# Optimization experiments

Measured on AMD Instinct MI355X. Metric: run time of the kernel, lower is better.

The kernel has to match this reference:

```python
import jax, jax.numpy as jnp
import numpy as np

N_NODES = 100000
N_EDGES = 1600000
IN_F, HID, N_COLORS = 128, 128, 10


def setup_inputs() -> dict:
    key = jax.random.key(0)
    k1, k2, k3, k4 = jax.random.split(key, 4)
    x = jax.random.normal(k1, (N_NODES, IN_F), dtype=jnp.float32)
    edge_index = jax.random.randint(k2, (2, N_EDGES), 0, N_NODES, dtype=jnp.int64)
    # Glorot-ish init for weights
    W1 = jax.random.normal(k3, (IN_F, HID), dtype=jnp.float32) / np.sqrt(IN_F)
    b1 = jnp.zeros((HID,), dtype=jnp.float32)
    W2 = jax.random.normal(k4, (HID, N_COLORS), dtype=jnp.float32) / np.sqrt(HID)
    b2 = jnp.zeros((N_COLORS,), dtype=jnp.float32)
    return {"x": x, "edge_index": edge_index, "W1": W1, "b1": b1, "W2": W2, "b2": b2}


def _gcn_norm(edge_index, num_nodes):
    # Add self-loops, compute symmetric normalization D^-1/2 (A+I) D^-1/2
    loops = jnp.arange(num_nodes, dtype=edge_index.dtype)
    src = jnp.concatenate([edge_index[0], loops])
    dst = jnp.concatenate([edge_index[1], loops])
    deg = jax.ops.segment_sum(jnp.ones_like(dst, dtype=jnp.float32), dst,
                              num_segments=num_nodes)
    deg_isqrt = jax.lax.rsqrt(deg)  # deg >= 1 due to self-loops
    norm = deg_isqrt[src] * deg_isqrt[dst]  # [E + N]
    return src, dst, norm


def _gcn_conv(h, src, dst, norm, num_nodes, W, b):
    # Linear transform first (PyG GCNConv), then gather-scale-scatter aggregate
    h = h @ W                                   # [N, out]
    msg = h[src] * norm[:, None]                # [E + N, out] gather
    out = jax.ops.segment_sum(msg, dst, num_segments=num_nodes)  # scatter-add
    return out + b


def reference(x, edge_index, W1, b1, W2, b2):
    n = x.shape[0]
    src, dst, norm = _gcn_norm(edge_index, n)
    h = _gcn_conv(x, src, dst, norm, n, W1, b1)
    h = jax.nn.relu(h)
    # dropout is identity in eval mode
    h = _gcn_conv(h, src, dst, norm, n, W2, b2)
    return jax.nn.softmax(h, axis=1)
```

## Files before the change

### kernel.cpp

```cpp
#include <hip/hip_runtime.h>
#include <hip/hip_fp16.h>

#define IN_F 128
#define HID  128
#define NC   10
#define H2P  16
#define NPB  128
#define NBMAX 784
#define BCAP 2560
#define CAPP 2944
#define EPB  4096
#define LDW  136

typedef _Float16 f16x8 __attribute__((ext_vector_type(8)));
typedef float f32x4 __attribute__((ext_vector_type(4)));
typedef int int4a __attribute__((ext_vector_type(4), aligned(4)));

__device__ inline __half2 shfl_xor_h2(__half2 v, int mask) {
    int i = __shfl_xor(*reinterpret_cast<int*>(&v), mask, 64);
    return *reinterpret_cast<__half2*>(&i);
}

__global__ __launch_bounds__(1024) void k_bin(const int* __restrict__ src,
                                              const int* __restrict__ dst,
                                              int* __restrict__ bcnt,
                                              unsigned int* __restrict__ binned,
                                              const float* __restrict__ W1,
                                              __half* __restrict__ WT,
                                              const float* __restrict__ W2,
                                              float* __restrict__ W2T,
                                              int E, int nbin) {
    __shared__ int hist[NBMAX];
    __shared__ int base[NBMAX];
    __shared__ int lofs[NBMAX];
    __shared__ int lcur[NBMAX];
    __shared__ int scan[1024];
    __shared__ unsigned int stage[EPB];
    __shared__ unsigned short sbin[EPB];
    const int tid = threadIdx.x;

    if (blockIdx.x == 0) {
        for (int i = tid; i < IN_F * HID; i += 1024) {
            int k = i >> 7, n = i & 127;
            WT[n * IN_F + k] = __float2half(W1[k * HID + n]);
        }
        for (int i = tid; i < NC * IN_F; i += 1024)
            W2T[i] = W2[(i & 127) * NC + (i >> 7)];
    }

    for (int b = tid; b < nbin; b += 1024) { hist[b] = 0; lcur[b] = 0; }
    __syncthreads();

    const int e0 = blockIdx.x * EPB + tid;
    int d[4], s[4];
    #pragma unroll
    for (int u = 0; u < 4; u++) {
        int e = e0 + u * 1024;
        d[u] = (e < E) ? dst[e] : -1;
        s[u] = (e < E) ? src[e] : 0;
        if (d[u] >= 0) atomicAdd(&hist[d[u] >> 7], 1);
    }
    __syncthreads();
    for (int b = tid; b < nbin; b += 1024) {
        int h = hist[b];
        base[b] = h ? atomicAdd(&bcnt[b], h) : 0;
    }
    scan[tid] = (tid < nbin) ? hist[tid] : 0;
    __syncthreads();
    for (int off = 1; off < 1024; off <<= 1) {
        int t = (tid >= off) ? scan[tid - off] : 0;
        __syncthreads();
        scan[tid] += t;
        __syncthreads();
    }
    if (tid < nbin) lofs[tid] = scan[tid] - hist[tid];
    __syncthreads();
    #pragma unroll
    for (int u = 0; u < 4; u++) {
        if (d[u] >= 0) {
            int b = d[u] >> 7;
            int slot = lofs[b] + atomicAdd(&lcur[b], 1);
            stage[slot] = ((unsigned)(d[u] & 127) << 17) | (unsigned)s[u];
            sbin[slot] = (unsigned short)b;
        }
    }
    __syncthreads();
    const int total = scan[1023];
    for (int i = tid; i < total; i += 1024) {
        int b = sbin[i];
        int o = base[b] + (i - lofs[b]);
        if (o < BCAP) binned[(size_t)b * BCAP + o] = stage[i];
    }
}

__global__ __launch_bounds__(512) void k_pg(const int* __restrict__ bcnt,
                                            const unsigned int* __restrict__ binned,
                                            int2* __restrict__ rowinfo,
                                            float* __restrict__ dis,
                                            int* __restrict__ csr,
                                            const float* __restrict__ X,
                                            const __half* __restrict__ WT,
                                            __half* __restrict__ hsh,
                                            __half* __restrict__ h2h,
                                            int N) {
    __shared__ int h[NPB];
    __shared__ int lb[NPB];
    __shared__ int cur[NPB];
    __shared__ float sdis[NPB];
    __shared__ int wtot[2];
    __shared__ _Float16 sX[2][32 * LDW];
    __shared__ _Float16 sW[128 * LDW];
    const int b = blockIdx.x;
    const int tid = threadIdx.x;

    if (tid < NPB) h[tid] = 0;
    __syncthreads();

    const int m = min(bcnt[b], BCAP);
    const unsigned int* p = binned + (size_t)b * BCAP;
    for (int i = tid; i < m; i += 512) atomicAdd(&h[p[i] >> 17], 1);
    __syncthreads();

    int myh = 0, cnt4 = 0;
    if (tid < NPB) { myh = h[tid]; cnt4 = (myh + 3) & ~3; }
    int inc = cnt4;
    if (tid < NPB) {
        #pragma unroll
        for (int off = 1; off < 64; off <<= 1) {
            int t = __shfl_up(inc, off, 64);
            if ((tid & 63) >= off) inc += t;
        }
        if ((tid & 63) == 63) wtot[tid >> 6] = inc;
    }
    __syncthreads();
    int ex = 0;
    if (tid < NPB) {
        ex = inc - cnt4 + ((tid >= 64) ? wtot[0] : 0);
        int node = b * NPB + tid;
        if (node < N) {
            rowinfo[node] = make_int2(b * CAPP + ex, cnt4);
            float dd = rsqrtf(1.0f + (float)myh);
            dis[node] = dd;
            sdis[tid] = dd;
        }
        lb[tid] = ex;
        cur[tid] = 0;
    }
    __syncthreads();
    for (int i = tid; i < m; i += 512) {
        unsigned v = p[i];
        int dl = v >> 17;
        int r = atomicAdd(&cur[dl], 1);
        csr[b * CAPP + lb[dl] + r] = (int)(v & 0x1FFFF);
    }
    if (tid < NPB) {
        for (int k = myh; k < cnt4; k++) csr[b * CAPP + ex + k] = N;
    }
    if (b == 0) {
        f16x8 z = {0, 0, 0, 0, 0, 0, 0, 0};
        if (tid < 16) *(f16x8*)(hsh + (size_t)N * HID + tid * 8) = z;
        if (tid < 2)  *(f16x8*)(h2h + (size_t)N * H2P + tid * 8) = z;
    }

    {
        int n = tid >> 2, part = tid & 3;
        const f16x8* srcp = (const f16x8*)(WT + n * IN_F);
        f16x8* dstp = (f16x8*)(sW + n * LDW);
        #pragma unroll
        for (int c = 0; c < 4; c++) dstp[part * 4 + c] = srcp[part * 4 + c];
    }

    const int wave = tid >> 6;
    const int grp  = wave >> 2;
    const int nbase = (wave & 3) * 32;
    const int lane = tid & 63;
    const int quad = lane >> 4;
    const int l16 = lane & 15;
    const int sub256 = tid >> 8;
    const int t256 = tid & 255;

    for (int t = 0; t < 2; t++) {
        __syncthreads();
        {
            int tdx = 2 * t + sub256;
            int r = t256 >> 3;
            int k0 = (t256 & 7) * 16;
            int row = b * NPB + tdx * 32 + r;
            if (row >= N) row = N - 1;
            const float* sp = X + (size_t)row * IN_F + k0;
            float4 f0 = *(const float4*)(sp);
            float4 f1 = *(const float4*)(sp + 4);
            float4 f2 = *(const float4*)(sp + 8);
            float4 f3 = *(const float4*)(sp + 12);
            f16x8 h0, h1;
            h0[0] = (_Float16)f0.x; h0[1] = (_Float16)f0.y;
            h0[2] = (_Float16)f0.z; h0[3] = (_Float16)f0.w;
            h0[4] = (_Float16)f1.x; h0[5] = (_Float16)f1.y;
            h0[6] = (_Float16)f1.z; h0[7] = (_Float16)f1.w;
            h1[0] = (_Float16)f2.x; h1[1] = (_Float16)f2.y;
            h1[2] = (_Float16)f2.z; h1[3] = (_Float16)f2.w;
            h1[4] = (_Float16)f3.x; h1[5] = (_Float16)f3.y;
            h1[6] = (_Float16)f3.z; h1[7] = (_Float16)f3.w;
            *(f16x8*)(sX[sub256] + r * LDW + k0) = h0;
            *(f16x8*)(sX[sub256] + r * LDW + k0 + 8) = h1;
        }
        __syncthreads();

        const int tdx = 2 * t + grp;
        f32x4 acc00 = {0,0,0,0}, acc01 = {0,0,0,0}, acc10 = {0,0,0,0}, acc11 = {0,0,0,0};
        #pragma unroll
        for (int kc = 0; kc < 4; kc++) {
            const int koff = kc * 32 + quad * 8;
            f16x8 a0 = *(const f16x8*)(sX[grp] + l16 * LDW + koff);
            f16x8 a1 = *(const f16x8*)(sX[grp] + (16 + l16) * LDW + koff);
            f16x8 b0 = *(const f16x8*)(sW + (nbase + l16) * LDW + koff);
            f16x8 b1 = *(const f16x8*)(sW + (nbase + 16 + l16) * LDW + koff);
            acc00 = __builtin_amdgcn_mfma_f32_16x16x32_f16(a0, b0, acc00, 0, 0, 0);
            acc01 = __builtin_amdgcn_mfma_f32_16x16x32_f16(a0, b1, acc01, 0, 0, 0);
            acc10 = __builtin_amdgcn_mfma_f32_16x16x32_f16(a1, b0, acc10, 0, 0, 0);
            acc11 = __builtin_amdgcn_mfma_f32_16x16x32_f16(a1, b1, acc11, 0, 0, 0);
        }
        #pragma unroll
        for (int r = 0; r < 4; r++) {
            {
                int lr = tdx * 32 + quad * 4 + r;
                int row = b * NPB + lr;
                if (row < N) {
                    float d = sdis[lr];
                    __half* o = hsh + (size_t)row * HID + nbase + l16;
                    o[0]  = __float2half(acc00[r] * d);
                    o[16] = __float2half(acc01[r] * d);
                }
            }
            {
                int lr = tdx * 32 + 16 + quad * 4 + r;
                int row = b * NPB + lr;
                if (row < N) {
                    float d = sdis[lr];
                    __half* o = hsh + (size_t)row * HID + nbase + l16;
                    o[0]  = __float2half(acc10[r] * d);
                    o[16] = __float2half(acc11[r] * d);
                }
            }
        }
    }
}

__global__ __launch_bounds__(256) void k_agg1(const __half* __restrict__ hsh,
                                              const int2* __restrict__ rowinfo,
                                              const int* __restrict__ csr,
                                              const float* __restrict__ dis,
                                              const float* __restrict__ b1,
                                              const float* __restrict__ W2T,
                                              __half* __restrict__ h2h,
                                              int N) {
    const int node = blockIdx.x * 4 + (threadIdx.x >> 6);
    if (node >= N) return;
    const int lane = threadIdx.x & 63;
    const int g   = lane >> 4;
    const int l16 = lane & 15;
    const int f0  = l16 * 8;
    const __half2 hz = __half2half2(__float2half(0.0f));

    const int2 ri = rowinfo[node];
    const int beg = ri.x, end = ri.x + ri.y;
    const float d = dis[node];

    __half2 acc2[4] = {hz, hz, hz, hz};
    if (g == 0) {
        float4 r = *(const float4*)(hsh + (size_t)node * HID + f0);
        const __half2* hh = (const __half2*)&r;
        acc2[0] = hh[0]; acc2[1] = hh[1]; acc2[2] = hh[2]; acc2[3] = hh[3];
    }

    int j0 = beg + 4 * g;
    if (j0 < end) {
        int4a cv0 = *(const int4a*)(csr + j0);
        int  j1 = j0 + 16;
        bool m1 = j1 < end;
        int4a cv1 = m1 ? *(const int4a*)(csr + j1) : cv0;
        float4 r0 = *(const float4*)(hsh + (size_t)cv0[0] * HID + f0);
        float4 r1 = *(const float4*)(hsh + (size_t)cv0[1] * HID + f0);
        float4 r2 = *(const float4*)(hsh + (size_t)cv0[2] * HID + f0);
        float4 r3 = *(const float4*)(hsh + (size_t)cv0[3] * HID + f0);
        while (true) {
            const int  j2 = j1 + 16;
            const bool m2 = m1 && (j2 < end);
            int4a cv2 = m2 ? *(const int4a*)(csr + j2) : cv1;
            float4 n0, n1, n2, n3;
            if (m1) {
                n0 = *(const float4*)(hsh + (size_t)cv1[0] * HID + f0);
                n1 = *(const float4*)(hsh + (size_t)cv1[1] * HID + f0);
                n2 = *(const float4*)(hsh + (size_t)cv1[2] * HID + f0);
                n3 = *(const float4*)(hsh + (size_t)cv1[3] * HID + f0);
            }
            const __half2* h0 = (const __half2*)&r0;
            const __half2* h1 = (const __half2*)&r1;
            const __half2* h2 = (const __half2*)&r2;
            const __half2* h3 = (const __half2*)&r3;
            #pragma unroll
            for (int i = 0; i < 4; i++) {
                acc2[i] = __hadd2(acc2[i], h0[i]);
                acc2[i] = __hadd2(acc2[i], h1[i]);
                acc2[i] = __hadd2(acc2[i], h2[i]);
                acc2[i] = __hadd2(acc2[i], h3[i]);
            }
            if (!m1) break;
            r0 = n0; r1 = n1; r2 = n2; r3 = n3;
            cv1 = cv2; m1 = m2; j1 = j2;
        }
    }

    #pragma unroll
    for (int i = 0; i < 4; i++) {
        acc2[i] = __hadd2(acc2[i], shfl_xor_h2(acc2[i], 16));
        acc2[i] = __hadd2(acc2[i], shfl_xor_h2(acc2[i], 32));
    }
    float acc[8];
    #pragma unroll
    for (int i = 0; i < 4; i++) {
        float2 t = __half22float2(acc2[i]);
        acc[2 * i] = t.x; acc[2 * i + 1] = t.y;
    }

    float4 ba = *(const float4*)(b1 + f0);
    float4 bb = *(const float4*)(b1 + f0 + 4);
    float h[8];
    h[0] = fmaxf(fmaf(d, acc[0], ba.x), 0.0f);
    h[1] = fmaxf(fmaf(d, acc[1], ba.y), 0.0f);
    h[2] = fmaxf(fmaf(d, acc[2], ba.z), 0.0f);
    h[3] = fmaxf(fmaf(d, acc[3], ba.w), 0.0f);
    h[4] = fmaxf(fmaf(d, acc[4], bb.x), 0.0f);
    h[5] = fmaxf(fmaf(d, acc[5], bb.y), 0.0f);
    h[6] = fmaxf(fmaf(d, acc[6], bb.z), 0.0f);
    h[7] = fmaxf(fmaf(d, acc[7], bb.w), 0.0f);

    const int cb = (g == 0) ? 0 : (g == 1) ? 3 : (g == 2) ? 6 : 8;
    const int nc = (g < 2) ? 3 : 2;
    float p[3];
    #pragma unroll
    for (int ci = 0; ci < 3; ci++) {
        if (ci < nc) {
            int c = cb + ci;
            float4 wa = *(const float4*)(W2T + c * IN_F + f0);
            float4 wb = *(const float4*)(W2T + c * IN_F + f0 + 4);
            float t = fmaf(h[0], wa.x, fmaf(h[1], wa.y, fmaf(h[2], wa.z, h[3] * wa.w)));
            t = fmaf(h[4], wb.x, fmaf(h[5], wb.y, fmaf(h[6], wb.z, fmaf(h[7], wb.w, t))));
            #pragma unroll
            for (int off = 1; off < 16; off <<= 1) t += __shfl_xor(t, off, 64);
            p[ci] = t;
        }
    }
    if (l16 == 0) {
        __half* o = h2h + (size_t)node * H2P + cb;
        for (int ci = 0; ci < nc; ci++) o[ci] = __float2half(d * p[ci]);
    }
}

__global__ __launch_bounds__(256) void k_agg2(const __half* __restrict__ h2h,
                                              const int2* __restrict__ rowinfo,
                                              const int* __restrict__ csr,
                                              const float* __restrict__ dis,
                                              const float* __restrict__ b2,
                                              float* __restrict__ out,
                                              int N) {
    int t = blockIdx.x * 256 + threadIdx.x;
    int node = t >> 3;
    if (node >= N) return;
    int o = t & 7;
    int q = o & 1;
    int eg = o >> 1;
    const int base = q * 8;
    const __half2 hz = __half2half2(__float2half(0.0f));

    __half2 a2[4] = {hz, hz, hz, hz};
    if (eg == 0) {
        float4 r = *(const float4*)(h2h + (size_t)node * H2P + base);
        const __half2* hh = (const __half2*)&r;
        a2[0] = hh[0]; a2[1] = hh[1]; a2[2] = hh[2]; a2[3] = hh[3];
    }
    const int2 ri = rowinfo[node];
    const int end = ri.x + ri.y;

    int j0 = ri.x + 4 * eg;
    if (j0 < end) {
        int4a cv0 = *(const int4a*)(csr + j0);
        int  j1 = j0 + 16;
        bool m1 = j1 < end;
        int4a cv1 = m1 ? *(const int4a*)(csr + j1) : cv0;
        float4 r0 = *(const float4*)(h2h + (size_t)cv0[0] * H2P + base);
        float4 r1 = *(const float4*)(h2h + (size_t)cv0[1] * H2P + base);
        float4 r2 = *(const float4*)(h2h + (size_t)cv0[2] * H2P + base);
        float4 r3 = *(const float4*)(h2h + (size_t)cv0[3] * H2P + base);
        while (true) {
            const int  j2 = j1 + 16;
            const bool m2 = m1 && (j2 < end);
            int4a cv2 = m2 ? *(const int4a*)(csr + j2) : cv1;
            float4 n0, n1, n2, n3;
            if (m1) {
                n0 = *(const float4*)(h2h + (size_t)cv1[0] * H2P + base);
                n1 = *(const float4*)(h2h + (size_t)cv1[1] * H2P + base);
                n2 = *(const float4*)(h2h + (size_t)cv1[2] * H2P + base);
                n3 = *(const float4*)(h2h + (size_t)cv1[3] * H2P + base);
            }
            const __half2* h0 = (const __half2*)&r0;
            const __half2* h1 = (const __half2*)&r1;
            const __half2* h2 = (const __half2*)&r2;
            const __half2* h3 = (const __half2*)&r3;
            #pragma unroll
            for (int i = 0; i < 4; i++) {
                a2[i] = __hadd2(a2[i], h0[i]);
                a2[i] = __hadd2(a2[i], h1[i]);
                a2[i] = __hadd2(a2[i], h2[i]);
                a2[i] = __hadd2(a2[i], h3[i]);
            }
            if (!m1) break;
            r0 = n0; r1 = n1; r2 = n2; r3 = n3;
            cv1 = cv2; m1 = m2; j1 = j2;
        }
    }

    #pragma unroll
    for (int i = 0; i < 4; i++) {
        a2[i] = __hadd2(a2[i], shfl_xor_h2(a2[i], 2));
        a2[i] = __hadd2(a2[i], shfl_xor_h2(a2[i], 4));
    }

    float a[8];
    #pragma unroll
    for (int i = 0; i < 4; i++) {
        float2 tt = __half22float2(a2[i]);
        a[2 * i] = tt.x; a[2 * i + 1] = tt.y;
    }

    const float d = dis[node];
    float vv[8];
    #pragma unroll
    for (int i = 0; i < 8; i++) {
        int f = base + i;
        vv[i] = (f < NC) ? fmaf(d, a[i], b2[f]) : -1e30f;
    }
    float m = vv[0];
    #pragma unroll
    for (int i = 1; i < 8; i++) m = fmaxf(m, vv[i]);
    m = fmaxf(m, __shfl_xor(m, 1, 64));
    float e[8];
    float s = 0.0f;
    #pragma unroll
    for (int i = 0; i < 8; i++) { e[i] = (base + i < NC) ? expf(vv[i] - m) : 0.0f; s += e[i]; }
    s += __shfl_xor(s, 1, 64);
    float inv = 1.0f / s;

    float* op = out + (size_t)node * NC;
    if (o == 0) {
        *(float2*)(op + 0) = make_float2(e[0] * inv, e[1] * inv);
        *(float2*)(op + 2) = make_float2(e[2] * inv, e[3] * inv);
        *(float2*)(op + 4) = make_float2(e[4] * inv, e[5] * inv);
        *(float2*)(op + 6) = make_float2(e[6] * inv, e[7] * inv);
    } else if (o == 1) {
        *(float2*)(op + 8) = make_float2(e[0] * inv, e[1] * inv);
    }
}

extern "C" void kernel_launch(void* const* d_in, const int* in_sizes, int n_in,
                              void* d_out, int out_size, void* d_ws, size_t ws_size,
                              hipStream_t stream) {
    const float* x  = (const float*)d_in[0];
    const int*   ei = (const int*)d_in[1];
    const float* W1 = (const float*)d_in[2];
    const float* b1 = (const float*)d_in[3];
    const float* W2 = (const float*)d_in[4];
    const float* b2 = (const float*)d_in[5];
    float* out = (float*)d_out;

    const int N = in_sizes[0] / IN_F;
    const int E = in_sizes[1] / 2;
    const int* esrc = ei;
    const int* edst = ei + E;
    const int nbin = (N + NPB - 1) / NPB;

    char* ws = (char*)d_ws;
    int2*   rowinfo = (int2*)(ws);
    float*  dis     = (float*)(ws + 0x100000);
    int*    bcnt    = (int*)(ws + 0x180000);
    __half* WT      = (__half*)(ws + 0x190000);
    float*  W2T     = (float*)(ws + 0x1A0000);
    unsigned int* binned = (unsigned int*)(ws + 0x200000);
    int*    csr     = (int*)(ws + 0xA00000);
    __half* hsh     = (__half*)(ws + 0x1400000);
    __half* h2h     = (__half*)(ws + 0x2D00000);

    hipMemsetAsync(bcnt, 0, (size_t)nbin * sizeof(int), stream);

    k_bin <<<(E + EPB - 1) / EPB, 1024, 0, stream>>>(esrc, edst, bcnt, binned, W1, WT, W2, W2T, E, nbin);
    k_pg  <<<nbin, 512, 0, stream>>>(bcnt, binned, rowinfo, dis, csr, x, WT, hsh, h2h, N);
    k_agg1<<<(N + 3) / 4, 256, 0, stream>>>(hsh, rowinfo, csr, dis, b1, W2T, h2h, N);
    k_agg2<<<(int)(((size_t)N * 8 + 255) / 256), 256, 0, stream>>>(h2h, rowinfo, csr, dis, b2, out, N);
}
```

Before: 224.5 us.

## Use wave-shuffle scan in binning and widen projection kernel to 1024 threads

In the binning kernel, the 1024-entry shared-memory Hillis-Steele scan with many barriers is replaced by a two-level wavefront shuffle scan. Edge indices are now loaded as int4 vectors with contiguous per-thread edges. The gather/projection kernel moves to 1024 threads per block, so all four 32-row X tiles are staged at once and the two-iteration loop with its barriers is removed. The binned entries are also kept in registers between the histogram and CSR-fill passes instead of being reloaded. The cost is a larger block, which raises per-block LDS and register use, lowers occupancy, and assumes at most 3072 entries per bin.

```diff
diff --git a/kernel.cpp b/kernel.cpp
--- a/kernel.cpp
+++ b/kernel.cpp
@@ -34,7 +34,7 @@
     __shared__ int base[NBMAX];
     __shared__ int lofs[NBMAX];
     __shared__ int lcur[NBMAX];
-    __shared__ int scan[1024];
+    __shared__ int wsum[16];
     __shared__ unsigned int stage[EPB];
     __shared__ unsigned short sbin[EPB];
     const int tid = threadIdx.x;
@@ -51,30 +51,52 @@
     for (int b = tid; b < nbin; b += 1024) { hist[b] = 0; lcur[b] = 0; }
     __syncthreads();
 
-    const int e0 = blockIdx.x * EPB + tid;
+    const int e0 = blockIdx.x * EPB + tid * 4;
     int d[4], s[4];
-    #pragma unroll
-    for (int u = 0; u < 4; u++) {
-        int e = e0 + u * 1024;
-        d[u] = (e < E) ? dst[e] : -1;
-        s[u] = (e < E) ? src[e] : 0;
+    if (e0 + 3 < E) {
+        int4a dv = *(const int4a*)(dst + e0);
+        int4a sv = *(const int4a*)(src + e0);
+        d[0] = dv[0]; d[1] = dv[1]; d[2] = dv[2]; d[3] = dv[3];
+        s[0] = sv[0]; s[1] = sv[1]; s[2] = sv[2]; s[3] = sv[3];
+    } else {
+        #pragma unroll
+        for (int u = 0; u < 4; u++) {
+            d[u] = (e0 + u < E) ? dst[e0 + u] : -1;
+            s[u] = (e0 + u < E) ? src[e0 + u] : 0;
+        }
+    }
+    #pragma unroll
+    for (int u = 0; u < 4; u++)
         if (d[u] >= 0) atomicAdd(&hist[d[u] >> 7], 1);
-    }
-    __syncthreads();
+    __syncthreads();
+
     for (int b = tid; b < nbin; b += 1024) {
         int h = hist[b];
         base[b] = h ? atomicAdd(&bcnt[b], h) : 0;
     }
-    scan[tid] = (tid < nbin) ? hist[tid] : 0;
-    __syncthreads();
-    for (int off = 1; off < 1024; off <<= 1) {
-        int t = (tid >= off) ? scan[tid - off] : 0;
-        __syncthreads();
-        scan[tid] += t;
-        __syncthreads();
-    }
-    if (tid < nbin) lofs[tid] = scan[tid] - hist[tid];
-    __syncthreads();
+    int v = (tid < nbin) ? hist[tid] : 0;
+    int inc = v;
+    #pragma unroll
+    for (int off = 1; off < 64; off <<= 1) {
+        int t = __shfl_up(inc, off, 64);
+        if ((tid & 63) >= off) inc += t;
+    }
+    if ((tid & 63) == 63) wsum[tid >> 6] = inc;
+    __syncthreads();
+    if (tid < 64) {
+        int wv = (tid < 16) ? wsum[tid] : 0;
+        int winc = wv;
+        #pragma unroll
+        for (int off = 1; off < 16; off <<= 1) {
+            int t = __shfl_up(winc, off, 64);
+            if (tid >= off) winc += t;
+        }
+        if (tid < 16) wsum[tid] = winc - wv;
+    }
+    __syncthreads();
+    if (tid < nbin) lofs[tid] = inc - v + wsum[tid >> 6];
+    __syncthreads();
+
     #pragma unroll
     for (int u = 0; u < 4; u++) {
         if (d[u] >= 0) {
@@ -85,7 +107,7 @@
         }
     }
     __syncthreads();
-    const int total = scan[1023];
+    const int total = lofs[nbin - 1] + hist[nbin - 1];
     for (int i = tid; i < total; i += 1024) {
         int b = sbin[i];
         int o = base[b] + (i - lofs[b]);
@@ -93,22 +115,22 @@
     }
 }
 
-__global__ __launch_bounds__(512) void k_pg(const int* __restrict__ bcnt,
-                                            const unsigned int* __restrict__ binned,
-                                            int2* __restrict__ rowinfo,
-                                            float* __restrict__ dis,
-                                            int* __restrict__ csr,
-                                            const float* __restrict__ X,
-                                            const __half* __restrict__ WT,
-                                            __half* __restrict__ hsh,
-                                            __half* __restrict__ h2h,
-                                            int N) {
+__global__ __launch_bounds__(1024) void k_pg(const int* __restrict__ bcnt,
+                                             const unsigned int* __restrict__ binned,
+                                             int2* __restrict__ rowinfo,
+                                             float* __restrict__ dis,
+                                             int* __restrict__ csr,
+                                             const float* __restrict__ X,
+                                             const __half* __restrict__ WT,
+                                             __half* __restrict__ hsh,
+                                             __half* __restrict__ h2h,
+                                             int N) {
     __shared__ int h[NPB];
     __shared__ int lb[NPB];
     __shared__ int cur[NPB];
     __shared__ float sdis[NPB];
     __shared__ int wtot[2];
-    __shared__ _Float16 sX[2][32 * LDW];
+    __shared__ _Float16 sX[4][32 * LDW];
     __shared__ _Float16 sW[128 * LDW];
     const int b = blockIdx.x;
     const int tid = threadIdx.x;
@@ -118,7 +140,11 @@
 
     const int m = min(bcnt[b], BCAP);
     const unsigned int* p = binned + (size_t)b * BCAP;
-    for (int i = tid; i < m; i += 512) atomicAdd(&h[p[i] >> 17], 1);
+    const int i0 = tid, i1 = tid + 1024, i2 = tid + 2048;
+    unsigned pv0 = 0, pv1 = 0, pv2 = 0;
+    if (i0 < m) { pv0 = p[i0]; atomicAdd(&h[pv0 >> 17], 1); }
+    if (i1 < m) { pv1 = p[i1]; atomicAdd(&h[pv1 >> 17], 1); }
+    if (i2 < m) { pv2 = p[i2]; atomicAdd(&h[pv2 >> 17], 1); }
     __syncthreads();
 
     int myh = 0, cnt4 = 0;
@@ -147,12 +173,9 @@
         cur[tid] = 0;
     }
     __syncthreads();
-    for (int i = tid; i < m; i += 512) {
-        unsigned v = p[i];
-        int dl = v >> 17;
-        int r = atomicAdd(&cur[dl], 1);
-        csr[b * CAPP + lb[dl] + r] = (int)(v & 0x1FFFF);
-    }
+    if (i0 < m) { int dl = pv0 >> 17; int r = atomicAdd(&cur[dl], 1); csr[b * CAPP + lb[dl] + r] = (int)(pv0 & 0x1FFFF); }
+    if (i1 < m) { int dl = pv1 >> 17; int r = atomicAdd(&cur[dl], 1); csr[b * CAPP + lb[dl] + r] = (int)(pv1 & 0x1FFFF); }
+    if (i2 < m) { int dl = pv2 >> 17; int r = atomicAdd(&cur[dl], 1); csr[b * CAPP + lb[dl] + r] = (int)(pv2 & 0x1FFFF); }
     if (tid < NPB) {
         for (int k = myh; k < cnt4; k++) csr[b * CAPP + ex + k] = N;
     }
@@ -163,12 +186,37 @@
     }
 
     {
-        int n = tid >> 2, part = tid & 3;
+        int n = tid >> 3, c = tid & 7;
         const f16x8* srcp = (const f16x8*)(WT + n * IN_F);
         f16x8* dstp = (f16x8*)(sW + n * LDW);
-        #pragma unroll
-        for (int c = 0; c < 4; c++) dstp[part * 4 + c] = srcp[part * 4 + c];
-    }
+        dstp[c]     = srcp[c];
+        dstp[c + 8] = srcp[c + 8];
+    }
+    {
+        const int sub = tid >> 8;
+        const int t256 = tid & 255;
+        const int r = t256 >> 3;
+        const int k0 = (t256 & 7) * 16;
+        int row = b * NPB + sub * 32 + r;
+        if (row >= N) row = N - 1;
+        const float* sp = X + (size_t)row * IN_F + k0;
+        float4 f0 = *(const float4*)(sp);
+        float4 f1 = *(const float4*)(sp + 4);
+        float4 f2 = *(const float4*)(sp + 8);
+        float4 f3 = *(const float4*)(sp + 12);
+        f16x8 h0, h1;
+        h0[0] = (_Float16)f0.x; h0[1] = (_Float16)f0.y;
+        h0[2] = (_Float16)f0.z; h0[3] = (_Float16)f0.w;
+        h0[4] = (_Float16)f1.x; h0[5] = (_Float16)f1.y;
+        h0[6] = (_Float16)f1.z; h0[7] = (_Float16)f1.w;
+        h1[0] = (_Float16)f2.x; h1[1] = (_Float16)f2.y;
+        h1[2] = (_Float16)f2.z; h1[3] = (_Float16)f2.w;
+        h1[4] = (_Float16)f3.x; h1[5] = (_Float16)f3.y;
+        h1[6] = (_Float16)f3.z; h1[7] = (_Float16)f3.w;
+        *(f16x8*)(sX[sub] + r * LDW + k0) = h0;
+        *(f16x8*)(sX[sub] + r * LDW + k0 + 8) = h1;
+    }
+    __syncthreads();
 
     const int wave = tid >> 6;
     const int grp  = wave >> 2;
@@ -176,71 +224,40 @@
     const int lane = tid & 63;
     const int quad = lane >> 4;
     const int l16 = lane & 15;
-    const int sub256 = tid >> 8;
-    const int t256 = tid & 255;
-
-    for (int t = 0; t < 2; t++) {
-        __syncthreads();
+
+    f32x4 acc00 = {0,0,0,0}, acc01 = {0,0,0,0}, acc10 = {0,0,0,0}, acc11 = {0,0,0,0};
+    #pragma unroll
+    for (int kc = 0; kc < 4; kc++) {
+        const int koff = kc * 32 + quad * 8;
+        f16x8 a0 = *(const f16x8*)(sX[grp] + l16 * LDW + koff);
+        f16x8 a1 = *(const f16x8*)(sX[grp] + (16 + l16) * LDW + koff);
+        f16x8 b0 = *(const f16x8*)(sW + (nbase + l16) * LDW + koff);
+        f16x8 b1 = *(const f16x8*)(sW + (nbase + 16 + l16) * LDW + koff);
+        acc00 = __builtin_amdgcn_mfma_f32_16x16x32_f16(a0, b0, acc00, 0, 0, 0);
+        acc01 = __builtin_amdgcn_mfma_f32_16x16x32_f16(a0, b1, acc01, 0, 0, 0);
+        acc10 = __builtin_amdgcn_mfma_f32_16x16x32_f16(a1, b0, acc10, 0, 0, 0);
+        acc11 = __builtin_amdgcn_mfma_f32_16x16x32_f16(a1, b1, acc11, 0, 0, 0);
+    }
+    #pragma unroll
+    for (int r = 0; r < 4; r++) {
         {
-            int tdx = 2 * t + sub256;
-            int r = t256 >> 3;
-            int k0 = (t256 & 7) * 16;
-            int row = b * NPB + tdx * 32 + r;
-            if (row >= N) row = N - 1;
-            const float* sp = X + (size_t)row * IN_F + k0;
-            float4 f0 = *(const float4*)(sp);
-            float4 f1 = *(const float4*)(sp + 4);
-            float4 f2 = *(const float4*)(sp + 8);
-            float4 f3 = *(const float4*)(sp + 12);
-            f16x8 h0, h1;
-            h0[0] = (_Float16)f0.x; h0[1] = (_Float16)f0.y;
-            h0[2] = (_Float16)f0.z; h0[3] = (_Float16)f0.w;
-            h0[4] = (_Float16)f1.x; h0[5] = (_Float16)f1.y;
-            h0[6] = (_Float16)f1.z; h0[7] = (_Float16)f1.w;
-            h1[0] = (_Float16)f2.x; h1[1] = (_Float16)f2.y;
-            h1[2] = (_Float16)f2.z; h1[3] = (_Float16)f2.w;
-            h1[4] = (_Float16)f3.x; h1[5] = (_Float16)f3.y;
-            h1[6] = (_Float16)f3.z; h1[7] = (_Float16)f3.w;
-            *(f16x8*)(sX[sub256] + r * LDW + k0) = h0;
-            *(f16x8*)(sX[sub256] + r * LDW + k0 + 8) = h1;
-        }
-        __syncthreads();
-
-        const int tdx = 2 * t + grp;
-        f32x4 acc00 = {0,0,0,0}, acc01 = {0,0,0,0}, acc10 = {0,0,0,0}, acc11 = {0,0,0,0};
-        #pragma unroll
-        for (int kc = 0; kc < 4; kc++) {
-            const int koff = kc * 32 + quad * 8;
-            f16x8 a0 = *(const f16x8*)(sX[grp] + l16 * LDW + koff);
-            f16x8 a1 = *(const f16x8*)(sX[grp] + (16 + l16) * LDW + koff);
-            f16x8 b0 = *(const f16x8*)(sW + (nbase + l16) * LDW + koff);
-            f16x8 b1 = *(const f16x8*)(sW + (nbase + 16 + l16) * LDW + koff);
-            acc00 = __builtin_amdgcn_mfma_f32_16x16x32_f16(a0, b0, acc00, 0, 0, 0);
-            acc01 = __builtin_amdgcn_mfma_f32_16x16x32_f16(a0, b1, acc01, 0, 0, 0);
-            acc10 = __builtin_amdgcn_mfma_f32_16x16x32_f16(a1, b0, acc10, 0, 0, 0);
-            acc11 = __builtin_amdgcn_mfma_f32_16x16x32_f16(a1, b1, acc11, 0, 0, 0);
-        }
-        #pragma unroll
-        for (int r = 0; r < 4; r++) {
-            {
-                int lr = tdx * 32 + quad * 4 + r;
-                int row = b * NPB + lr;
-                if (row < N) {
-                    float d = sdis[lr];
-                    __half* o = hsh + (size_t)row * HID + nbase + l16;
-                    o[0]  = __float2half(acc00[r] * d);
-                    o[16] = __float2half(acc01[r] * d);
-                }
+            int lr = grp * 32 + quad * 4 + r;
+            int row = b * NPB + lr;
+            if (row < N) {
+                float d = sdis[lr];
+                __half* o = hsh + (size_t)row * HID + nbase + l16;
+                o[0]  = __float2half(acc00[r] * d);
+                o[16] = __float2half(acc01[r] * d);
             }
-            {
-                int lr = tdx * 32 + 16 + quad * 4 + r;
-                int row = b * NPB + lr;
-                if (row < N) {
-                    float d = sdis[lr];
-                    __half* o = hsh + (size_t)row * HID + nbase + l16;
-                    o[0]  = __float2half(acc10[r] * d);
-                    o[16] = __float2half(acc11[r] * d);
-                }
+        }
+        {
+            int lr = grp * 32 + 16 + quad * 4 + r;
+            int row = b * NPB + lr;
+            if (row < N) {
+                float d = sdis[lr];
+                __half* o = hsh + (size_t)row * HID + nbase + l16;
+                o[0]  = __float2half(acc10[r] * d);
+                o[16] = __float2half(acc11[r] * d);
             }
         }
     }
@@ -493,7 +510,7 @@
     hipMemsetAsync(bcnt, 0, (size_t)nbin * sizeof(int), stream);
 
     k_bin <<<(E + EPB - 1) / EPB, 1024, 0, stream>>>(esrc, edst, bcnt, binned, W1, WT, W2, W2T, E, nbin);
-    k_pg  <<<nbin, 512, 0, stream>>>(bcnt, binned, rowinfo, dis, csr, x, WT, hsh, h2h, N);
+    k_pg  <<<nbin, 1024, 0, stream>>>(bcnt, binned, rowinfo, dis, csr, x, WT, hsh, h2h, N);
     k_agg1<<<(N + 3) / 4, 256, 0, stream>>>(hsh, rowinfo, csr, dis, b1, W2T, h2h, N);
     k_agg2<<<(int)(((size_t)N * 8 + 255) / 256), 256, 0, stream>>>(h2h, rowinfo, csr, dis, b2, out, N);
 }
```

Measured after the change: 221.6 us. No clear change (-1.3%).
